# Kernel optimization log

Hardware: AMD Instinct MI355X
Metric: run time of the kernel (lower is better)

## Reference

```python
import jax, jax.numpy as jnp
import numpy as np

H = 16
W = 16
THRESH = 1.0
B = 32

# NOTE: [5.0, 1.0] reproduces the (likely buggy) constant in the original source.
SRC_POINTS = jnp.array([[0.0,0.0],[0.5,0.0],[1.0,0.0],[0.0,0.5],[0.5,0.5],[1.0,0.5],[0.0,1.0],[5.0,1.0],[1.0,1.0]], dtype=jnp.float32)

def _conv(x, w, stride, padding):
    return jax.lax.conv_general_dilated(x, w, (stride, stride), padding, dimension_numbers=('NHWC', 'HWIO', 'NHWC'))

def _tps_u(r):
    return r * r * jnp.log(r + 1e-6)

def _pdist(a, b):
    # a [...,2], b [n,2] -> [..., n] euclidean distances (eps for sqrt-at-0 safety)
    return jnp.sqrt(jnp.sum((a[..., None, :] - b) ** 2, axis=-1) + 1e-12)

def _tps_fit(ctrl, values):
    # cheind/py-thin-plate-spline TPS.fit with reduced=True. ctrl [n,2], values [n] -> theta [n+2]
    n = ctrl.shape[0]
    K = _tps_u(_pdist(ctrl, ctrl))
    P = jnp.concatenate([jnp.ones((n, 1), ctrl.dtype), ctrl], axis=1)
    A = jnp.zeros((n + 3, n + 3), ctrl.dtype)
    A = A.at[:n, :n].set(K).at[:n, n:].set(P).at[n:, :n].set(P.T)
    v = jnp.zeros(n + 3, ctrl.dtype).at[:n].set(values)
    theta = jnp.linalg.solve(A, v)
    return theta[1:]

def _tps_z(pts, ctrl, theta):
    # pts [m,2], theta reduced [n+2] -> [m]
    U = _tps_u(_pdist(pts, ctrl))
    w, a = theta[:-3], theta[-3:]
    w = jnp.concatenate([-jnp.sum(w, keepdims=True), w])
    return U @ w + a[0] + pts[:, 0] * a[1] + pts[:, 1] * a[2]

def _inlier_mask(geo):
    # geo [18] -> mask [H, W, H, W], mask[a_y, a_x, b_y, b_x]
    mv = geo.reshape(9, 2)
    dst = SRC_POINTS + mv
    delta = SRC_POINTS - dst  # c_src - c_dst (tps_theta_from_points)
    th_x = _tps_fit(dst, delta[:, 0])
    th_y = _tps_fit(dst, delta[:, 1])
    xs = jnp.linspace(0.0, 1.0, W)
    ys = jnp.linspace(0.0, 1.0, H)
    gx, gy = jnp.meshgrid(xs, ys)  # [H, W], gx varies along b_x
    pts = jnp.stack([gx.ravel(), gy.ravel()], axis=-1)
    ax = (gx + _tps_z(pts, dst, th_x).reshape(H, W)) * (H - 1)  # grid[...,0]*(map_size[0]-1)
    ay = (gy + _tps_z(pts, dst, th_y).reshape(H, W)) * (W - 1)
    # integer x in [ceil(ax-t), floor(ax+t)] clipped to [0,W-1]  <=>  |x - ax| <= t for x in range
    ix = jnp.arange(W, dtype=ax.dtype)
    iy = jnp.arange(H, dtype=ay.dtype)
    mx = jnp.abs(ix[:, None, None] - ax[None]) <= THRESH  # [W(a_x), H(b_y), W(b_x)]
    my = jnp.abs(iy[:, None, None] - ay[None]) <= THRESH  # [H(a_y), H(b_y), W(b_x)]
    return (my[:, None] & mx[None]).astype(jnp.float32)   # [H, W, H, W]

def _forward(image_A, image_B, W1, W2, W3, W4, Wr1, Wr2, Wd, bd):
    def feat(img):
        x = jax.nn.relu(_conv(img, W1, 2, 'SAME'))   # 256 -> 128
        x = jax.nn.relu(_conv(x, W2, 2, 'SAME'))     # 128 -> 64
        x = jax.nn.relu(_conv(x, W3, 2, 'SAME'))     # 64 -> 32
        x = jax.nn.relu(_conv(x, W4, 2, 'SAME'))     # 32 -> 16
        return x / (jnp.linalg.norm(x, axis=-1, keepdims=True) + 1e-6)  # channelwise l2 norm
    fA = feat(image_A)
    fB = feat(image_B)
    corr = jnp.einsum('bijc,bklc->bijkl', fA, fB)    # [B, H, W, H, W]
    b = corr.shape[0]
    r = corr.reshape(b, H, W, H * W)
    r = jax.nn.relu(_conv(r, Wr1, 1, 'VALID'))       # 16 -> 10
    r = jax.nn.relu(_conv(r, Wr2, 1, 'VALID'))       # 10 -> 6
    geo = r.reshape(b, -1) @ Wd + bd                 # [B, 18]
    # tf.numpy_function blocks gradients -> stop_gradient on the mask path
    masks = jax.lax.stop_gradient(jax.vmap(_inlier_mask)(geo))
    return jnp.sum(corr * masks, axis=(1, 2, 3, 4))  # [B]

def setup_inputs():
    key = jax.random.key(0)
    ks = jax.random.split(key, 10)
    s = 0.05
    return {
        'image_A': jax.random.normal(ks[0], (B, 256, 256, 3), jnp.float32),
        'image_B': jax.random.normal(ks[1], (B, 256, 256, 3), jnp.float32),
        'W1': jax.random.normal(ks[2], (3, 3, 3, 64), jnp.float32) * s,
        'W2': jax.random.normal(ks[3], (3, 3, 64, 128), jnp.float32) * s,
        'W3': jax.random.normal(ks[4], (3, 3, 128, 256), jnp.float32) * s,
        'W4': jax.random.normal(ks[5], (3, 3, 256, 512), jnp.float32) * s,
        'Wr1': jax.random.normal(ks[6], (7, 7, 256, 128), jnp.float32) * s,
        'Wr2': jax.random.normal(ks[7], (5, 5, 128, 64), jnp.float32) * s,
        'Wd': jax.random.normal(ks[8], (2304, 18), jnp.float32) * s,
        'bd': jnp.zeros((18,), jnp.float32),
    }

def reference(image_A, image_B, W1, W2, W3, W4, Wr1, Wr2, Wd, bd):
    return _forward(image_A, image_B, W1, W2, W3, W4, Wr1, Wr2, Wd, bd)
```

## Files before the change

kernel.cpp:

```cpp
#include <hip/hip_runtime.h>
#include <math.h>


typedef __attribute__((ext_vector_type(8))) _Float16 f16x8;
typedef __attribute__((ext_vector_type(4))) float f32x4;

__device__ __forceinline__ unsigned short f2h(float f) {
  return __builtin_bit_cast(unsigned short, (_Float16)f);
}
__device__ __forceinline__ float h2f(unsigned short u) {
  return (float)__builtin_bit_cast(_Float16, u);
}

__global__ __launch_bounds__(256) void wt_single(const float* __restrict__ w,
                                                 unsigned short* __restrict__ wt,
                                                 int K, int C) {
  const int idx = blockIdx.x * 256 + threadIdx.x;
  if (idx < K * C) {
    const int k = idx / C, o = idx % C;
    wt[(size_t)o * K + k] = f2h(w[idx]);
  }
}

__global__ __launch_bounds__(256) void wt1_prep(const float* __restrict__ w,
                                                unsigned short* __restrict__ wt) {
  const int idx = blockIdx.x * 256 + threadIdx.x;
  if (idx < 2048) {
    const int o = idx >> 5, k = idx & 31;
    wt[idx] = (k < 27) ? f2h(w[(size_t)k * 64 + o]) : (unsigned short)0;
  }
}

__global__ __launch_bounds__(256) void conv1_mfma(const float* __restrict__ in,
                                                  const unsigned short* __restrict__ wt1,
                                                  unsigned short* __restrict__ out) {
  const int i = blockIdx.x;
  const int b = blockIdx.y;
  const int tid = threadIdx.x;
  const int lane = tid & 63, wid = tid >> 6;
  const int lrow = lane & 15, quad = lane >> 4;

  __shared__ _Float16 Rows[3][771];

  const float* __restrict__ inb = in + (size_t)b * 196608;
#pragma unroll
  for (int di = 0; di < 3; ++di) {
    const int y = 2 * i + di;
    if (y < 256) {
      const float* __restrict__ row = inb + (size_t)y * 768;
      for (int e = tid; e < 768; e += 256) Rows[di][e] = (_Float16)row[e];
    } else {
      for (int e = tid; e < 768; e += 256) Rows[di][e] = (_Float16)0.f;
    }
    if (tid < 3) Rows[di][768 + tid] = (_Float16)0.f;
  }
  __syncthreads();

  f16x8 bf[4];
#pragma unroll
  for (int ni = 0; ni < 4; ++ni)
    bf[ni] = *(const f16x8*)(wt1 + (ni * 16 + lrow) * 32 + quad * 8);

  f16x8 af[2];
#pragma unroll
  for (int mi = 0; mi < 2; ++mi) {
    const int j = wid * 32 + mi * 16 + lrow;
#pragma unroll
    for (int s = 0; s < 8; ++s) {
      const int k = quad * 8 + s;
      if (k < 27) {
        const int di = k / 9, dj = (k / 3) % 3, c = k % 3;
        af[mi][s] = Rows[di][(2 * j + dj) * 3 + c];
      } else {
        af[mi][s] = (_Float16)0.f;
      }
    }
  }

  f32x4 acc[2][4];
#pragma unroll
  for (int mi = 0; mi < 2; ++mi)
#pragma unroll
    for (int ni = 0; ni < 4; ++ni) {
      const f32x4 z = {0.f, 0.f, 0.f, 0.f};
      acc[mi][ni] = __builtin_amdgcn_mfma_f32_16x16x32_f16(af[mi], bf[ni], z, 0, 0, 0);
    }

  unsigned short* __restrict__ ob = out + (((size_t)b * 128 + i) * 128) * 64;
#pragma unroll
  for (int mi = 0; mi < 2; ++mi)
#pragma unroll
    for (int ni = 0; ni < 4; ++ni)
#pragma unroll
      for (int r = 0; r < 4; ++r) {
        const int j = wid * 32 + mi * 16 + quad * 4 + r;
        const int col = ni * 16 + lrow;
        ob[(size_t)j * 64 + col] = f2h(fmaxf(acc[mi][ni][r], 0.f));
      }
}

template <int BM, int BN, int CIN, int COUT, int KH, int KW, int STRIDE,
          int SAMEPAD, int SPLIT, int SK, int BATB, int OUTF32, int RELU>
__global__ __launch_bounds__(256) void tile_conv(
    const unsigned short* __restrict__ in, const unsigned short* __restrict__ wt,
    unsigned short* __restrict__ outh, float* __restrict__ outf,
    int Hin, int Win, int Hout, int Wout, int aLo, int bLo) {
  constexpr int LDA = 72;
  constexpr int CPT = CIN / 64;
  constexpr int LA = BM / 32;
  constexpr int LB = BN / 32;
  constexpr int KTOT = KH * KW * CIN;
  constexpr int MT = BM / 32;
  constexpr int NT = BN / 32;
  __shared__ _Float16 As[2][(1 + SPLIT) * BM * LDA];
  __shared__ _Float16 Bs[2][(1 + SPLIT) * BN * LDA];

  const int t = threadIdx.x;
  const int lane = t & 63, wid = t >> 6;
  const int lrow = lane & 15, quad = lane >> 4;
  const int m0 = blockIdx.x * BM;
  const int n0 = blockIdx.y * BN;

  int pixB[LA], iS[LA], jS[LA], lofA[LA];
#pragma unroll
  for (int i = 0; i < LA; ++i) {
    const int u = t + 256 * i;
    const int r = u >> 3, sl = u & 7;
    const int m = m0 + r;
    const int j = m % Wout;
    const int t2 = m / Wout;
    const int ii = t2 % Hout;
    const int b = t2 / Hout;
    iS[i] = ii * STRIDE;
    jS[i] = j * STRIDE;
    pixB[i] = ((b * Hin + iS[i]) * Win + jS[i]) * CIN + sl * 8;
    lofA[i] = r * LDA + sl * 8;
  }
  const unsigned short* wb = wt;
  if (BATB) wb += (size_t)(m0 / (Hout * Wout)) * COUT * KTOT;
  int bofB[LB], lofB[LB];
#pragma unroll
  for (int i = 0; i < LB; ++i) {
    const int u = t + 256 * i;
    const int r = u >> 3, sl = u & 7;
    bofB[i] = (n0 + r) * KTOT + sl * 8;
    lofB[i] = r * LDA + sl * 8;
  }

  const f16x8 zh = {0, 0, 0, 0, 0, 0, 0, 0};
  f32x4 acc[MT][NT];
#pragma unroll
  for (int mi = 0; mi < MT; ++mi)
#pragma unroll
    for (int ni = 0; ni < NT; ++ni) acc[mi][ni] = {0.f, 0.f, 0.f, 0.f};

  const int mB = (wid >> 1) * (BM / 2);
  const int nB = (wid & 1) * (BN / 2);

  int tap_lo = 0, tap_hi = KH * KW;
  if (SK > 1) {
    tap_lo = (int)blockIdx.z * KH * KW / SK;
    tap_hi = ((int)blockIdx.z + 1) * KH * KW / SK;
  }
  const int ch_lo = tap_lo * CPT, ch_hi = tap_hi * CPT;

  f16x8 va[LA], vb[LB], va2[LA], vb2[LB];

  auto load_ch = [&](int ch) {
    const int tap = ch / CPT;
    const int c0 = (ch % CPT) * 64;
    const int di = tap / KW, dj = tap % KW;
    const int toff = (di * Win + dj) * CIN + c0;
    const int woff = tap * CIN + c0;
#pragma unroll
    for (int i = 0; i < LA; ++i) {
      const bool ok = !SAMEPAD || ((iS[i] + di < Hin) && (jS[i] + dj < Win));
      va[i] = ok ? *(const f16x8*)(in + pixB[i] + toff) : zh;
      if (SPLIT) va2[i] = ok ? *(const f16x8*)(in + pixB[i] + toff + aLo) : zh;
    }
#pragma unroll
    for (int i = 0; i < LB; ++i) {
      vb[i] = *(const f16x8*)(wb + bofB[i] + woff);
      if (SPLIT) vb2[i] = *(const f16x8*)(wb + bofB[i] + woff + bLo);
    }
  };
  auto write_buf = [&](int buf) {
#pragma unroll
    for (int i = 0; i < LA; ++i) {
      *(f16x8*)&As[buf][lofA[i]] = va[i];
      if (SPLIT) *(f16x8*)&As[buf][BM * LDA + lofA[i]] = va2[i];
    }
#pragma unroll
    for (int i = 0; i < LB; ++i) {
      *(f16x8*)&Bs[buf][lofB[i]] = vb[i];
      if (SPLIT) *(f16x8*)&Bs[buf][BN * LDA + lofB[i]] = vb2[i];
    }
  };

  load_ch(ch_lo);
  write_buf(0);
  int cur = 0;
  for (int ch = ch_lo; ch < ch_hi; ++ch) {
    const bool hasNext = (ch + 1 < ch_hi);
    if (hasNext) load_ch(ch + 1);
    __syncthreads();
#pragma unroll
    for (int ks = 0; ks < 2; ++ks) {
      f16x8 af[MT], bf[NT], al[MT], bl[NT];
#pragma unroll
      for (int mi = 0; mi < MT; ++mi) {
        const int off = (mB + mi * 16 + lrow) * LDA + ks * 32 + quad * 8;
        af[mi] = *(const f16x8*)&As[cur][off];
        if (SPLIT) al[mi] = *(const f16x8*)&As[cur][BM * LDA + off];
      }
#pragma unroll
      for (int ni = 0; ni < NT; ++ni) {
        const int off = (nB + ni * 16 + lrow) * LDA + ks * 32 + quad * 8;
        bf[ni] = *(const f16x8*)&Bs[cur][off];
        if (SPLIT) bl[ni] = *(const f16x8*)&Bs[cur][BN * LDA + off];
      }
#pragma unroll
      for (int mi = 0; mi < MT; ++mi)
#pragma unroll
        for (int ni = 0; ni < NT; ++ni) {
          if (SPLIT) {
            acc[mi][ni] = __builtin_amdgcn_mfma_f32_16x16x32_f16(af[mi], bl[ni],
                                                                 acc[mi][ni], 0, 0, 0);
            acc[mi][ni] = __builtin_amdgcn_mfma_f32_16x16x32_f16(al[mi], bf[ni],
                                                                 acc[mi][ni], 0, 0, 0);
          }
          acc[mi][ni] = __builtin_amdgcn_mfma_f32_16x16x32_f16(af[mi], bf[ni],
                                                               acc[mi][ni], 0, 0, 0);
        }
    }
    if (hasNext) write_buf(cur ^ 1);
    cur ^= 1;
  }
  const size_t slice =
      (SK > 1) ? (size_t)blockIdx.z * ((size_t)gridDim.x * BM * COUT) : 0;
#pragma unroll
  for (int mi = 0; mi < MT; ++mi)
#pragma unroll
    for (int ni = 0; ni < NT; ++ni)
#pragma unroll
      for (int r = 0; r < 4; ++r) {
        const int row = m0 + mB + mi * 16 + quad * 4 + r;
        const int col = n0 + nB + ni * 16 + lrow;
        const size_t idx = (size_t)row * COUT + col;
        float v = acc[mi][ni][r];
        if (SK > 1) {
          outf[slice + idx] = v;
        } else if (OUTF32) {
          outf[idx] = v;
          outh[idx] = f2h(v);
        } else {
          if (RELU) v = fmaxf(v, 0.f);
          outh[idx] = f2h(v);
        }
      }
}

template <int MT, int NT, int CIN, int COUT, int KH, int KW, int SK>
__global__ __launch_bounds__(256) void gemm_conv(
    const unsigned short* __restrict__ in, const unsigned short* __restrict__ wt,
    float* __restrict__ outf, int Hin, int Win, int Hout, int Wout) {
  const int KTOT = KH * KW * CIN;
  const int lane = threadIdx.x & 63;
  const int wid = threadIdx.x >> 6;
  const int lrow = lane & 15;
  const int quad = lane >> 4;
  const int m0 = (blockIdx.x * 4 + wid) * (16 * MT);
  const int n0 = blockIdx.y * (16 * NT);

  int pix[MT];
#pragma unroll
  for (int mi = 0; mi < MT; ++mi) {
    const int m = m0 + mi * 16 + lrow;
    const int j = m % Wout;
    const int t = m / Wout;
    const int i = t % Hout;
    const int b = t / Hout;
    pix[mi] = (b * Hin + i) * Win + j;
  }
  const unsigned short* brow[NT];
#pragma unroll
  for (int ni = 0; ni < NT; ++ni)
    brow[ni] = wt + (size_t)(n0 + ni * 16 + lrow) * KTOT + quad * 8;

  f32x4 acc[MT][NT];
#pragma unroll
  for (int mi = 0; mi < MT; ++mi)
#pragma unroll
    for (int ni = 0; ni < NT; ++ni) acc[mi][ni] = {0.f, 0.f, 0.f, 0.f};

  const int tap_lo = (int)blockIdx.z * KH * KW / SK;
  const int tap_hi = ((int)blockIdx.z + 1) * KH * KW / SK;
  for (int tap = tap_lo; tap < tap_hi; ++tap) {
    const int di = tap / KW, dj = tap % KW;
    const unsigned short* ap[MT];
#pragma unroll
    for (int mi = 0; mi < MT; ++mi)
      ap[mi] = in + ((size_t)pix[mi] + di * Win + dj) * CIN + quad * 8;
    const int ko = tap * CIN;
#pragma unroll
    for (int c0 = 0; c0 < CIN; c0 += 32) {
      f16x8 ah[MT], bh[NT];
#pragma unroll
      for (int mi = 0; mi < MT; ++mi) ah[mi] = *(const f16x8*)(ap[mi] + c0);
#pragma unroll
      for (int ni = 0; ni < NT; ++ni) bh[ni] = *(const f16x8*)(brow[ni] + ko + c0);
#pragma unroll
      for (int mi = 0; mi < MT; ++mi)
#pragma unroll
        for (int ni = 0; ni < NT; ++ni)
          acc[mi][ni] = __builtin_amdgcn_mfma_f32_16x16x32_f16(ah[mi], bh[ni],
                                                               acc[mi][ni], 0, 0, 0);
    }
  }
  const size_t slice = (size_t)blockIdx.z * ((size_t)gridDim.x * 64 * MT * COUT);
#pragma unroll
  for (int mi = 0; mi < MT; ++mi)
#pragma unroll
    for (int ni = 0; ni < NT; ++ni)
#pragma unroll
      for (int r = 0; r < 4; ++r) {
        const int row = m0 + mi * 16 + quad * 4 + r;
        const int col = n0 + ni * 16 + lrow;
        outf[slice + (size_t)row * COUT + col] = acc[mi][ni][r];
      }
}

__global__ __launch_bounds__(256) void sum_relu_s(const float* __restrict__ p,
                                                  unsigned short* __restrict__ o,
                                                  int n, int parts) {
  const int idx = blockIdx.x * 256 + threadIdx.x;
  if (idx < n) {
    float v = 0.f;
    for (int s = 0; s < parts; ++s) v += p[(size_t)s * n + idx];
    o[idx] = f2h(fmaxf(v, 0.f));
  }
}
__global__ __launch_bounds__(256) void sum_relu_f(const float* __restrict__ p,
                                                  float* __restrict__ o,
                                                  int n, int parts) {
  const int idx = blockIdx.x * 256 + threadIdx.x;
  if (idx < n) {
    float v = 0.f;
    for (int s = 0; s < parts; ++s) v += p[(size_t)s * n + idx];
    o[idx] = fmaxf(v, 0.f);
  }
}

__global__ __launch_bounds__(64) void l2norm_k(const unsigned short* __restrict__ x,
                                               unsigned short* __restrict__ y,
                                               int loOff) {
  const int lane = threadIdx.x;
  const f16x8 v = *(const f16x8*)(x + (size_t)blockIdx.x * 512 + lane * 8);
  float f[8];
  float s = 0.f;
#pragma unroll
  for (int k = 0; k < 8; ++k) {
    f[k] = (float)v[k];
    s += f[k] * f[k];
  }
#pragma unroll
  for (int off = 32; off; off >>= 1) s += __shfl_xor(s, off, 64);
  const float inv = 1.f / (sqrtf(s) + 1e-6f);
  f16x8 vh, vl;
#pragma unroll
  for (int k = 0; k < 8; ++k) {
    const float nv = f[k] * inv;
    const _Float16 hi = (_Float16)nv;
    vh[k] = hi;
    vl[k] = (_Float16)(nv - (float)hi);
  }
  unsigned short* ph = y + (size_t)blockIdx.x * 512 + lane * 8;
  *(f16x8*)ph = vh;
  *(f16x8*)(ph + (size_t)loOff) = vl;
}

__global__ __launch_bounds__(64) void dense_k(const float* __restrict__ r2,
                                              const float* __restrict__ wd,
                                              const float* __restrict__ bd,
                                              float* __restrict__ geo) {
  const int o = blockIdx.x;
  const int b = blockIdx.y;
  const int lane = threadIdx.x;
  const float* __restrict__ rb = r2 + (size_t)b * 2304;
  float s = 0.f;
  for (int k = lane; k < 2304; k += 64) s += rb[k] * wd[(size_t)k * 18 + o];
#pragma unroll
  for (int off = 32; off; off >>= 1) s += __shfl_xor(s, off, 64);
  if (lane == 0) geo[b * 18 + o] = s + bd[o];
}

__device__ __forceinline__ float tps_u(float r) { return r * r * logf(r + 1e-6f); }

__global__ __launch_bounds__(64) void tps_k(const float* __restrict__ geo,
                                            float* __restrict__ axb,
                                            float* __restrict__ ayb) {
  const int b = blockIdx.x;
  const int tid = threadIdx.x;
  __shared__ float M[12][14];
  __shared__ float fel[12];
  __shared__ float dxs[9], dys[9];
  __shared__ float th[2][12];
  __shared__ float sW[2][9];
  __shared__ float sA[2][3];
  __shared__ int sPiv;

  const float srcx[9] = {0.f, 0.5f, 1.f, 0.f, 0.5f, 1.f, 0.f, 5.f, 1.f};
  const float srcy[9] = {0.f, 0.f, 0.f, 0.5f, 0.5f, 0.5f, 1.f, 1.f, 1.f};

  if (tid < 9) {
    const float mx = geo[b * 18 + 2 * tid], my = geo[b * 18 + 2 * tid + 1];
    dxs[tid] = srcx[tid] + mx;
    dys[tid] = srcy[tid] + my;
    M[tid][12] = -mx;
    M[tid][13] = -my;
  } else if (tid < 12) {
    M[tid][12] = 0.f;
    M[tid][13] = 0.f;
  }
  __syncthreads();
  for (int e = tid; e < 81; e += 64) {
    const int p = e / 9, q = e % 9;
    const float ddx = dxs[p] - dxs[q], ddy = dys[p] - dys[q];
    const float r = sqrtf(ddx * ddx + ddy * ddy + 1e-12f);
    M[p][q] = tps_u(r);
  }
  if (tid < 9) {
    M[tid][9] = 1.f;  M[tid][10] = dxs[tid]; M[tid][11] = dys[tid];
    M[9][tid] = 1.f;  M[10][tid] = dxs[tid]; M[11][tid] = dys[tid];
  } else if (tid < 12) {
    M[tid][9] = 0.f; M[tid][10] = 0.f; M[tid][11] = 0.f;
  }
  __syncthreads();

  for (int k = 0; k < 12; ++k) {
    if (tid == 0) {
      int piv = k;
      float best = fabsf(M[k][k]);
      for (int r = k + 1; r < 12; ++r) {
        const float v = fabsf(M[r][k]);
        if (v > best) { best = v; piv = r; }
      }
      sPiv = piv;
    }
    __syncthreads();
    const int piv = sPiv;
    if (piv != k && tid < 14) {
      const float tmp = M[k][tid];
      M[k][tid] = M[piv][tid];
      M[piv][tid] = tmp;
    }
    __syncthreads();
    if (tid > k && tid < 12) fel[tid] = M[tid][k] / M[k][k];
    __syncthreads();
    for (int e = tid; e < (11 - k) * 14; e += 64) {
      const int r = k + 1 + e / 14, cc = e % 14;
      if (cc >= k) M[r][cc] -= fel[r] * M[k][cc];
    }
    __syncthreads();
  }

  const int grp = tid >> 4;
  const int cc = tid & 15;
  for (int k = 11; k >= 0; --k) {
    float prod = 0.f;
    if (grp < 2 && cc > k && cc < 12) prod = M[k][cc] * th[grp][cc];
#pragma unroll
    for (int off = 8; off; off >>= 1) prod += __shfl_xor(prod, off, 16);
    if (grp < 2 && cc == 0) th[grp][k] = (M[k][12 + grp] - prod) / M[k][k];
    __syncthreads();
  }

  if (tid < 2) {
    float sw = 0.f;
    for (int p = 1; p < 9; ++p) {
      sW[tid][p] = th[tid][p];
      sw += th[tid][p];
    }
    sW[tid][0] = -sw;
    sA[tid][0] = th[tid][9];
    sA[tid][1] = th[tid][10];
    sA[tid][2] = th[tid][11];
  }
  __syncthreads();

  for (int p = tid; p < 256; p += 64) {
    const int pi = p >> 4, pj = p & 15;
    const float x = pj * (1.f / 15.f), y = pi * (1.f / 15.f);
    float zx = sA[0][0] + x * sA[0][1] + y * sA[0][2];
    float zy = sA[1][0] + x * sA[1][1] + y * sA[1][2];
#pragma unroll
    for (int c = 0; c < 9; ++c) {
      const float ddx = x - dxs[c], ddy = y - dys[c];
      const float r = sqrtf(ddx * ddx + ddy * ddy + 1e-12f);
      const float u = tps_u(r);
      zx += u * sW[0][c];
      zy += u * sW[1][c];
    }
    axb[b * 256 + p] = (x + zx) * 15.f;
    ayb[b * 256 + p] = (y + zy) * 15.f;
  }
}

__global__ __launch_bounds__(256) void masksum_k(const float* __restrict__ corr,
                                                 const float* __restrict__ axb,
                                                 const float* __restrict__ ayb,
                                                 float* __restrict__ out) {
  const int b = blockIdx.x;
  const int pB = threadIdx.x;
  const float ax = axb[b * 256 + pB];
  const float ay = ayb[b * 256 + pB];
  const float* __restrict__ cb = corr + (size_t)b * 65536;
  float s = 0.f;
  for (int i = 0; i < 16; ++i) {
    if (fabsf((float)i - ay) <= 1.0f) {
      const float* __restrict__ ci = cb + (size_t)i * 16 * 256 + pB;
      for (int j = 0; j < 16; ++j) {
        if (fabsf((float)j - ax) <= 1.0f) s += ci[(size_t)j * 256];
      }
    }
  }
  __shared__ float sm[256];
  sm[pB] = s;
  __syncthreads();
  for (int off = 128; off; off >>= 1) {
    if (pB < off) sm[pB] += sm[pB + off];
    __syncthreads();
  }
  if (pB == 0) out[b] = sm[0];
}

extern "C" void kernel_launch(void* const* d_in, const int* in_sizes, int n_in,
                              void* d_out, int out_size, void* d_ws, size_t ws_size,
                              hipStream_t stream) {
  const float* imgA = (const float*)d_in[0];
  const float* imgB = (const float*)d_in[1];
  const float* W1 = (const float*)d_in[2];
  const float* W2 = (const float*)d_in[3];
  const float* W3 = (const float*)d_in[4];
  const float* W4 = (const float*)d_in[5];
  const float* Wr1 = (const float*)d_in[6];
  const float* Wr2 = (const float*)d_in[7];
  const float* Wd = (const float*)d_in[8];
  const float* bd = (const float*)d_in[9];

  float* ws = (float*)d_ws;
  unsigned short* WT2 = (unsigned short*)(ws + 0);
  unsigned short* WT3 = (unsigned short*)(ws + 36864);
  unsigned short* WT4 = (unsigned short*)(ws + 184320);
  unsigned short* WTr1 = (unsigned short*)(ws + 774144);
  unsigned short* WTr2 = (unsigned short*)(ws + 1576960);
  unsigned short* FEATs = (unsigned short*)(ws + 1679360);
  unsigned short* S2 = (unsigned short*)(ws + 5873664);
  unsigned short* S1 = (unsigned short*)(ws + 14262272);
  unsigned short* S3 = (unsigned short*)(ws + 14262272);
  unsigned short* FEATsp = (unsigned short*)(ws + 5873664);
  float* CORRf = ws + 14262272;
  unsigned short* CORRh = (unsigned short*)(ws + 16359424);
  float* R1p = ws + 17408000;
  unsigned short* R1h = (unsigned short*)(ws + 20275200);
  float* R2p = ws + 20480000;
  float* R2f = ws + 22323200;
  float* GEOb = ws + 22396928;
  float* AXb = ws + 22397504;
  float* AYb = ws + 22405696;
  unsigned short* WT1 = (unsigned short*)(ws + 31039488);

  wt1_prep<<<8, 256, 0, stream>>>(W1, WT1);
  wt_single<<<288, 256, 0, stream>>>(W2, WT2, 576, 128);
  wt_single<<<1152, 256, 0, stream>>>(W3, WT3, 1152, 256);
  wt_single<<<4608, 256, 0, stream>>>(W4, WT4, 2304, 512);
  wt_single<<<6272, 256, 0, stream>>>(Wr1, WTr1, 12544, 128);
  wt_single<<<800, 256, 0, stream>>>(Wr2, WTr2, 3200, 64);

  for (int img = 0; img < 2; ++img) {
    const float* src = img ? imgB : imgA;
    conv1_mfma<<<dim3(128, 32), 256, 0, stream>>>(src, WT1, S1);
    tile_conv<128, 128, 64, 128, 3, 3, 2, 1, 0, 1, 0, 0, 1>
        <<<dim3(1024, 1), 256, 0, stream>>>(S1, WT2, S2, nullptr,
                                            128, 128, 64, 64, 0, 0);
    tile_conv<128, 128, 128, 256, 3, 3, 2, 1, 0, 1, 0, 0, 1>
        <<<dim3(256, 2), 256, 0, stream>>>(S2, WT3, S3, nullptr,
                                           64, 64, 32, 32, 0, 0);
    tile_conv<64, 128, 256, 512, 3, 3, 2, 1, 0, 1, 0, 0, 1>
        <<<dim3(128, 4), 256, 0, stream>>>(S3, WT4, FEATs + (size_t)img * 4194304,
                                           nullptr, 32, 32, 16, 16, 0, 0);
  }

  l2norm_k<<<16384, 64, 0, stream>>>(FEATs, FEATsp, 8388608);
  tile_conv<64, 64, 512, 256, 1, 1, 1, 0, 1, 1, 1, 1, 0>
      <<<dim3(128, 4), 256, 0, stream>>>(FEATsp, FEATsp + 4194304, CORRh, CORRf,
                                         16, 16, 16, 16, 8388608, 8388608);
  tile_conv<64, 128, 256, 128, 7, 7, 1, 0, 0, 7, 0, 0, 0>
      <<<dim3(50, 1, 7), 256, 0, stream>>>(CORRh, WTr1, nullptr, R1p,
                                           16, 16, 10, 10, 0, 0);
  sum_relu_s<<<1600, 256, 0, stream>>>(R1p, R1h, 409600, 7);
  gemm_conv<1, 4, 128, 64, 5, 5, 25>
      <<<dim3(18, 1, 25), 256, 0, stream>>>(R1h, WTr2, R2p, 10, 10, 6, 6);
  sum_relu_f<<<288, 256, 0, stream>>>(R2p, R2f, 73728, 25);
  dense_k<<<dim3(18, 32), 64, 0, stream>>>(R2f, Wd, bd, GEOb);
  tps_k<<<32, 64, 0, stream>>>(GEOb, AXb, AYb);
  masksum_k<<<32, 256, 0, stream>>>(CORRf, AXb, AYb, (float*)d_out);
}
```

Measured before the change: 473.0 us.

## Load conv tiles directly into LDS with XOR-swizzled unpadded layout

Replaces the register-staged global-to-shared copy in tile_conv with 16-byte global_load_lds direct-to-LDS loads. The padded LDS rows (stride 72) become unpadded rows with an XOR swizzle, applied on the global read side and undone in the fragment reads, to avoid bank conflicts. Out-of-bounds padding taps now read from a zero-filled buffer instead of selecting a zero register. This is meant to remove register pressure and the VGPR round-trip for staging, and to let prefetch overlap compute. It relies on the barrier waiting for outstanding async LDS loads.

```diff
diff --git a/kernel.cpp b/kernel.cpp
--- a/kernel.cpp
+++ b/kernel.cpp
@@ -10,6 +10,12 @@
 }
 __device__ __forceinline__ float h2f(unsigned short u) {
   return (float)__builtin_bit_cast(_Float16, u);
+}
+
+__device__ __forceinline__ void gl16(const unsigned short* g, _Float16* l) {
+  auto* gp = (const __attribute__((address_space(1))) unsigned int*)(g);
+  auto* lp = (__attribute__((address_space(3))) unsigned int*)(l);
+  __builtin_amdgcn_global_load_lds(gp, lp, 16, 0, 0);
 }
 
 __global__ __launch_bounds__(256) void wt_single(const float* __restrict__ w,
@@ -29,6 +35,11 @@
     const int o = idx >> 5, k = idx & 31;
     wt[idx] = (k < 27) ? f2h(w[(size_t)k * 64 + o]) : (unsigned short)0;
   }
+}
+
+__global__ __launch_bounds__(256) void zero_fill(float* __restrict__ p, int n) {
+  const int i = blockIdx.x * 256 + threadIdx.x;
+  if (i < n) p[i] = 0.f;
 }
 
 __global__ __launch_bounds__(256) void conv1_mfma(const float* __restrict__ in,
@@ -104,16 +115,17 @@
 __global__ __launch_bounds__(256) void tile_conv(
     const unsigned short* __restrict__ in, const unsigned short* __restrict__ wt,
     unsigned short* __restrict__ outh, float* __restrict__ outf,
+    const unsigned short* __restrict__ zp,
     int Hin, int Win, int Hout, int Wout, int aLo, int bLo) {
-  constexpr int LDA = 72;
   constexpr int CPT = CIN / 64;
   constexpr int LA = BM / 32;
   constexpr int LB = BN / 32;
   constexpr int KTOT = KH * KW * CIN;
   constexpr int MT = BM / 32;
   constexpr int NT = BN / 32;
-  __shared__ _Float16 As[2][(1 + SPLIT) * BM * LDA];
-  __shared__ _Float16 Bs[2][(1 + SPLIT) * BN * LDA];
+  constexpr int PL = 1 + SPLIT;
+  __shared__ _Float16 As[2][PL * BM * 64];
+  __shared__ _Float16 Bs[2][PL * BN * 64];
 
   const int t = threadIdx.x;
   const int lane = t & 63, wid = t >> 6;
@@ -121,11 +133,12 @@
   const int m0 = blockIdx.x * BM;
   const int n0 = blockIdx.y * BN;
 
-  int pixB[LA], iS[LA], jS[LA], lofA[LA];
+  const int q8 = ((t & 7) ^ ((t >> 3) & 7)) * 8;
+
+  int pixB[LA], iS[LA], jS[LA];
 #pragma unroll
   for (int i = 0; i < LA; ++i) {
-    const int u = t + 256 * i;
-    const int r = u >> 3, sl = u & 7;
+    const int r = (t >> 3) + 32 * i;
     const int m = m0 + r;
     const int j = m % Wout;
     const int t2 = m / Wout;
@@ -133,21 +146,17 @@
     const int b = t2 / Hout;
     iS[i] = ii * STRIDE;
     jS[i] = j * STRIDE;
-    pixB[i] = ((b * Hin + iS[i]) * Win + jS[i]) * CIN + sl * 8;
-    lofA[i] = r * LDA + sl * 8;
+    pixB[i] = ((b * Hin + iS[i]) * Win + jS[i]) * CIN + q8;
   }
   const unsigned short* wb = wt;
   if (BATB) wb += (size_t)(m0 / (Hout * Wout)) * COUT * KTOT;
-  int bofB[LB], lofB[LB];
+  int bofB[LB];
 #pragma unroll
   for (int i = 0; i < LB; ++i) {
-    const int u = t + 256 * i;
-    const int r = u >> 3, sl = u & 7;
-    bofB[i] = (n0 + r) * KTOT + sl * 8;
-    lofB[i] = r * LDA + sl * 8;
-  }
-
-  const f16x8 zh = {0, 0, 0, 0, 0, 0, 0, 0};
+    const int r = (t >> 3) + 32 * i;
+    bofB[i] = (n0 + r) * KTOT + q8;
+  }
+
   f32x4 acc[MT][NT];
 #pragma unroll
   for (int mi = 0; mi < MT; ++mi)
@@ -164,9 +173,7 @@
   }
   const int ch_lo = tap_lo * CPT, ch_hi = tap_hi * CPT;
 
-  f16x8 va[LA], vb[LB], va2[LA], vb2[LB];
-
-  auto load_ch = [&](int ch) {
+  auto stage = [&](int buf, int ch) {
     const int tap = ch / CPT;
     const int c0 = (ch % CPT) * 64;
     const int di = tap / KW, dj = tap % KW;
@@ -175,49 +182,42 @@
 #pragma unroll
     for (int i = 0; i < LA; ++i) {
       const bool ok = !SAMEPAD || ((iS[i] + di < Hin) && (jS[i] + dj < Win));
-      va[i] = ok ? *(const f16x8*)(in + pixB[i] + toff) : zh;
-      if (SPLIT) va2[i] = ok ? *(const f16x8*)(in + pixB[i] + toff + aLo) : zh;
+      const unsigned short* s0 = ok ? in + pixB[i] + toff : zp + q8;
+      gl16(s0, &As[buf][t * 8 + 2048 * i]);
+      if (SPLIT) {
+        const unsigned short* s1 = ok ? in + pixB[i] + toff + aLo : zp + q8;
+        gl16(s1, &As[buf][BM * 64 + t * 8 + 2048 * i]);
+      }
     }
 #pragma unroll
     for (int i = 0; i < LB; ++i) {
-      vb[i] = *(const f16x8*)(wb + bofB[i] + woff);
-      if (SPLIT) vb2[i] = *(const f16x8*)(wb + bofB[i] + woff + bLo);
+      gl16(wb + bofB[i] + woff, &Bs[buf][t * 8 + 2048 * i]);
+      if (SPLIT)
+        gl16(wb + bofB[i] + woff + bLo, &Bs[buf][BN * 64 + t * 8 + 2048 * i]);
     }
   };
-  auto write_buf = [&](int buf) {
-#pragma unroll
-    for (int i = 0; i < LA; ++i) {
-      *(f16x8*)&As[buf][lofA[i]] = va[i];
-      if (SPLIT) *(f16x8*)&As[buf][BM * LDA + lofA[i]] = va2[i];
-    }
-#pragma unroll
-    for (int i = 0; i < LB; ++i) {
-      *(f16x8*)&Bs[buf][lofB[i]] = vb[i];
-      if (SPLIT) *(f16x8*)&Bs[buf][BN * LDA + lofB[i]] = vb2[i];
-    }
-  };
-
-  load_ch(ch_lo);
-  write_buf(0);
+
+  stage(0, ch_lo);
   int cur = 0;
   for (int ch = ch_lo; ch < ch_hi; ++ch) {
-    const bool hasNext = (ch + 1 < ch_hi);
-    if (hasNext) load_ch(ch + 1);
     __syncthreads();
+    if (ch + 1 < ch_hi) stage(cur ^ 1, ch + 1);
 #pragma unroll
     for (int ks = 0; ks < 2; ++ks) {
       f16x8 af[MT], bf[NT], al[MT], bl[NT];
 #pragma unroll
       for (int mi = 0; mi < MT; ++mi) {
-        const int off = (mB + mi * 16 + lrow) * LDA + ks * 32 + quad * 8;
+        const int row = mB + mi * 16 + lrow;
+        const int off = row * 64 + (((ks * 4 + quad) ^ (row & 7)) * 8);
         af[mi] = *(const f16x8*)&As[cur][off];
-        if (SPLIT) al[mi] = *(const f16x8*)&As[cur][BM * LDA + off];
+        if (SPLIT) al[mi] = *(const f16x8*)&As[cur][BM * 64 + off];
       }
 #pragma unroll
       for (int ni = 0; ni < NT; ++ni) {
-        const int off = (nB + ni * 16 + lrow) * LDA + ks * 32 + quad * 8;
+        const int row = nB + ni * 16 + lrow;
+        const int off = row * 64 + (((ks * 4 + quad) ^ (row & 7)) * 8);
         bf[ni] = *(const f16x8*)&Bs[cur][off];
-        if (SPLIT) bl[ni] = *(const f16x8*)&Bs[cur][BN * LDA + off];
+        if (SPLIT) bl[ni] = *(const f16x8*)&Bs[cur][BN * 64 + off];
       }
 #pragma unroll
       for (int mi = 0; mi < MT; ++mi)
@@ -233,7 +233,6 @@
                                                                acc[mi][ni], 0, 0, 0);
         }
     }
-    if (hasNext) write_buf(cur ^ 1);
     cur ^= 1;
   }
   const size_t slice =
@@ -569,7 +568,10 @@
   float* AXb = ws + 22397504;
   float* AYb = ws + 22405696;
   unsigned short* WT1 = (unsigned short*)(ws + 31039488);
-
+  float* ZPf = ws + 31040512;
+  const unsigned short* ZP = (const unsigned short*)ZPf;
+
+  zero_fill<<<4, 256, 0, stream>>>(ZPf, 1024);
   wt1_prep<<<8, 256, 0, stream>>>(W1, WT1);
   wt_single<<<288, 256, 0, stream>>>(W2, WT2, 576, 128);
   wt_single<<<1152, 256, 0, stream>>>(W3, WT3, 1152, 256);
@@ -581,22 +583,22 @@
     const float* src = img ? imgB : imgA;
     conv1_mfma<<<dim3(128, 32), 256, 0, stream>>>(src, WT1, S1);
     tile_conv<128, 128, 64, 128, 3, 3, 2, 1, 0, 1, 0, 0, 1>
-        <<<dim3(1024, 1), 256, 0, stream>>>(S1, WT2, S2, nullptr,
+        <<<dim3(1024, 1), 256, 0, stream>>>(S1, WT2, S2, nullptr, ZP,
                                             128, 128, 64, 64, 0, 0);
     tile_conv<128, 128, 128, 256, 3, 3, 2, 1, 0, 1, 0, 0, 1>
-        <<<dim3(256, 2), 256, 0, stream>>>(S2, WT3, S3, nullptr,
+        <<<dim3(256, 2), 256, 0, stream>>>(S2, WT3, S3, nullptr, ZP,
                                            64, 64, 32, 32, 0, 0);
     tile_conv<64, 128, 256, 512, 3, 3, 2, 1, 0, 1, 0, 0, 1>
         <<<dim3(128, 4), 256, 0, stream>>>(S3, WT4, FEATs + (size_t)img * 4194304,
-                                           nullptr, 32, 32, 16, 16, 0, 0);
+                                           nullptr, ZP, 32, 32, 16, 16, 0, 0);
   }
 
   l2norm_k<<<16384, 64, 0, stream>>>(FEATs, FEATsp, 8388608);
   tile_conv<64, 64, 512, 256, 1, 1, 1, 0, 1, 1, 1, 1, 0>
       <<<dim3(128, 4), 256, 0, stream>>>(FEATsp, FEATsp + 4194304, CORRh, CORRf,
-                                         16, 16, 16, 16, 8388608, 8388608);
+                                         ZP, 16, 16, 16, 16, 8388608, 8388608);
   tile_conv<64, 128, 256, 128, 7, 7, 1, 0, 0, 7, 0, 0, 0>
-      <<<dim3(50, 1, 7), 256, 0, stream>>>(CORRh, WTr1, nullptr, R1p,
+      <<<dim3(50, 1, 7), 256, 0, stream>>>(CORRh, WTr1, nullptr, R1p, ZP,
                                            16, 16, 10, 10, 0, 0);
   sum_relu_s<<<1600, 256, 0, stream>>>(R1p, R1h, 409600, 7);
   gemm_conv<1, 4, 128, 64, 5, 5, 25>
```

Result: slower. 498.2 us (+5.3%).
